# Kernel tuning notes

Measured on AMD Instinct MI355X. Metric: run time of the kernel, lower is better.

Reference implementation:

```python
import jax, jax.numpy as jnp
import numpy as np

EPS = 1e-3  # keras LayerNormalization default epsilon

def _layernorm(x, g, b):
    mu = jnp.mean(x, axis=-1, keepdims=True)
    var = jnp.mean(jnp.square(x - mu), axis=-1, keepdims=True)
    return (x - mu) * jax.lax.rsqrt(var + EPS) * g + b

def setup_inputs() -> dict:
    key = jax.random.key(0)
    ks = jax.random.split(key, 12)
    B, T, C = 2, 2048, 768
    s = 0.02
    return {
        "x": jax.random.normal(ks[0], (B, T, C), jnp.float32),
        "ln1_g": jnp.ones((C,), jnp.float32), "ln1_b": jnp.zeros((C,), jnp.float32),
        "Wq": jax.random.normal(ks[1], (C, C), jnp.float32) * s, "bq": jnp.zeros((C,), jnp.float32),
        "Wk": jax.random.normal(ks[2], (C, C), jnp.float32) * s, "bk": jnp.zeros((C,), jnp.float32),
        "Wv": jax.random.normal(ks[3], (C, C), jnp.float32) * s, "bv": jnp.zeros((C,), jnp.float32),
        "ln2_g": jnp.ones((C,), jnp.float32), "ln2_b": jnp.zeros((C,), jnp.float32),
        "W1": jax.random.normal(ks[4], (C, 4 * C), jnp.float32) * s, "b1": jnp.zeros((4 * C,), jnp.float32),
        "W2": jax.random.normal(ks[5], (4 * C, C), jnp.float32) * s, "b2": jnp.zeros((C,), jnp.float32),
    }

def reference(x, ln1_g, ln1_b, Wq, bq, Wk, bk, Wv, bv, ln2_g, ln2_b, W1, b1, W2, b2):
    H = 12
    B, T, C = x.shape
    dh = C // H
    # pre-LN (note: original overwrites x with LN output before residual)
    x = _layernorm(x, ln1_g, ln1_b)
    q = (x @ Wq + bq).reshape(B, T, H, dh).transpose(0, 2, 1, 3)
    k = (x @ Wk + bk).reshape(B, T, H, dh).transpose(0, 2, 1, 3)
    v = (x @ Wv + bv).reshape(B, T, H, dh).transpose(0, 2, 1, 3)
    # original computes K @ Q^T (transpose_b on query)
    scores = jnp.einsum('bhid,bhjd->bhij', k, q) / jnp.sqrt(jnp.float32(dh))
    mask = jnp.tril(jnp.ones((T, T), bool))
    scores = jnp.where(mask, scores, -jnp.inf)
    p = jax.nn.softmax(scores, axis=-1)
    y = jnp.einsum('bhij,bhjd->bhid', p, v)  # [B,H,T,dh]
    y = y.transpose(0, 2, 1, 3).reshape(B, T, C)
    x = x + y
    h = _layernorm(x, ln2_g, ln2_b)
    h = jax.nn.gelu(h @ W1 + b1, approximate=False)
    h = h @ W2 + b2
    return x + h
```

## Files before the change

### kernel.cpp

```cpp
#include <hip/hip_runtime.h>
#include <hip/hip_bf16.h>
#include <cmath>


#define BB 2
#define TT 2048
#define CC 768
#define HH 12
#define DH 64
#define NROWS (BB*TT)
#define NHEADS (BB*HH)

typedef __attribute__((ext_vector_type(8))) short bf16x8;
typedef __attribute__((ext_vector_type(4))) float f32x4;
typedef __attribute__((ext_vector_type(4))) unsigned short u16x4;

__device__ __forceinline__ unsigned short f2bf(float f){
  union { __hip_bfloat16 h; unsigned short u; } c;
  c.h = __float2bfloat16(f);
  return c.u;
}
__device__ __forceinline__ float bf2f(unsigned short u){
  union { unsigned int i; float f; } x; x.i = ((unsigned int)u) << 16; return x.f;
}
template<int BK>
__device__ __forceinline__ int swzk(int r, int c){
  if constexpr (BK == 64) return (r << 6) + (c ^ ((r & 7) << 3));
  else                    return (r << 5) + (c ^ (((r >> 1) & 3) << 3));
}
template<int BK>
__device__ __forceinline__ int swzsrc(int r, int c){
  if constexpr (BK == 64) return c ^ ((r & 7) << 3);
  else                    return c ^ (((r >> 1) & 3) << 3);
}
__device__ __forceinline__ float wred_sum(float v){
  #pragma unroll
  for(int m = 1; m < 64; m <<= 1) v += __shfl_xor(v, m, 64);
  return v;
}
__device__ __forceinline__ float gelu_fast(float x){
  float x2 = x * x;
  float e = x * fmaf(x2, 0.044715f, 1.0f) * 2.30203136f;
  float t = exp2f(e);
  return x - x / (t + 1.0f);
}
__device__ __forceinline__ void gload_lds16(const void* g, void* l){
  __builtin_amdgcn_global_load_lds((const __attribute__((address_space(1))) void*)g,
                                   (__attribute__((address_space(3))) void*)l, 16, 0, 0);
}
template<int N> __device__ __forceinline__ void waitcnt_vm(){
  if constexpr (N == 0)      asm volatile("s_waitcnt vmcnt(0)" ::: "memory");
  else if constexpr (N == 4) asm volatile("s_waitcnt vmcnt(4)" ::: "memory");
  else if constexpr (N == 8) asm volatile("s_waitcnt vmcnt(8)" ::: "memory");
  else static_assert(N == 0 || N == 4 || N == 8, "unsupported vmcnt");
}

#define SCLOG2 (0.125f * 1.44269504f)

__device__ __forceinline__ void tc_body(const float* __restrict__ in,
                                        unsigned short* __restrict__ out,
                                        int K, int N, int bx, int by,
                                        float (*tile)[33]){
  int n0 = bx * 32, k0 = by * 32;
  int t = threadIdx.x;
  int r = t >> 3, c4 = (t & 7) * 4;
  *(float4*)&tile[r][c4] = *(const float4*)&in[(size_t)(k0 + r) * N + n0 + c4];
  __syncthreads();
  u16x4 pk;
  #pragma unroll
  for(int j = 0; j < 4; j++) pk[j] = f2bf(tile[c4 + j][r]);
  *(u16x4*)&out[(size_t)(n0 + r) * K + k0 + c4] = pk;
}

__device__ __forceinline__ void ln_body(const float* __restrict__ in,
                                        const float* __restrict__ gm,
                                        const float* __restrict__ bt,
                                        unsigned short* __restrict__ out_b,
                                        int r){
  int t = threadIdx.x;
  const float* row = in + (size_t)r * CC;
  float v0 = row[t], v1 = row[t + 256], v2 = row[t + 512];
  float s = wred_sum(v0 + v1 + v2);
  __shared__ float red[4];
  if((t & 63) == 0) red[t >> 6] = s;
  __syncthreads();
  float mu = (red[0] + red[1] + red[2] + red[3]) * (1.0f / CC);
  float d0 = v0 - mu, d1 = v1 - mu, d2 = v2 - mu;
  float q = wred_sum(d0 * d0 + d1 * d1 + d2 * d2);
  __shared__ float red2[4];
  if((t & 63) == 0) red2[t >> 6] = q;
  __syncthreads();
  float var = (red2[0] + red2[1] + red2[2] + red2[3]) * (1.0f / CC);
  float rinv = rsqrtf(var + 1e-3f);
  float o0 = d0 * rinv * gm[t]       + bt[t];
  float o1 = d1 * rinv * gm[t + 256] + bt[t + 256];
  float o2 = d2 * rinv * gm[t + 512] + bt[t + 512];
  size_t base = (size_t)r * CC;
  out_b[base + t] = f2bf(o0); out_b[base + t + 256] = f2bf(o1); out_b[base + t + 512] = f2bf(o2);
}

__global__ __launch_bounds__(256) void prep_ln_kernel(const float* __restrict__ Wq,
                                                      const float* __restrict__ Wk,
                                                      const float* __restrict__ Wv,
                                                      const float* __restrict__ W1,
                                                      const float* __restrict__ W2,
                                                      const float* __restrict__ bq,
                                                      const float* __restrict__ bk,
                                                      const float* __restrict__ bv,
                                                      const float* __restrict__ x,
                                                      const float* __restrict__ ln1g,
                                                      const float* __restrict__ ln1b,
                                                      unsigned short* __restrict__ wqkv,
                                                      unsigned short* __restrict__ w1t,
                                                      unsigned short* __restrict__ w2t,
                                                      float* __restrict__ bqkv,
                                                      unsigned short* __restrict__ xlnb){
  __shared__ float tile[32][33];
  int o = blockIdx.x;
  if(o < 1728){
    int z = o / 576, r = o % 576;
    const float* in = (z == 0) ? Wq : (z == 1) ? Wk : Wv;
    tc_body(in, wqkv + (size_t)z * CC * CC, CC, CC, r % 24, r / 24, tile);
  } else if(o < 4032){
    int r = o - 1728;
    tc_body(W1, w1t, CC, 4 * CC, r % 96, r / 96, tile);
  } else if(o < 6336){
    int r = o - 4032;
    tc_body(W2, w2t, 4 * CC, CC, r % 24, r / 24, tile);
  } else if(o < 6345){
    int i = (o - 6336) * 256 + threadIdx.x;
    if(i < 3 * CC) bqkv[i] = (i < CC) ? bq[i] : (i < 2 * CC) ? bk[i - CC] : bv[i - 2 * CC];
  } else {
    ln_body(x, ln1g, ln1b, xlnb, o - 6345);
  }
}

template<int MODE, int TILE, int BK>
__global__ __launch_bounds__(256) void gemm_bt(const unsigned short* __restrict__ A,
                                               const unsigned short* __restrict__ Bt,
                                               const float* __restrict__ bias,
                                               const float* __restrict__ resid,
                                               void* __restrict__ outp,
                                               unsigned short* __restrict__ vt,
                                               int M, int N, int K){
  constexpr int F = TILE / 32;
  constexpr int SEGS = TILE * BK / 512;
  constexpr int R = SEGS / 4;
  constexpr int NLD = 2 * R;
  constexpr int LPR = BK / 8;
  constexpr int RPS = 512 / BK;
  __shared__ unsigned short As[3][TILE * BK];
  __shared__ unsigned short Bs[3][TILE * BK];
  int nb = gridDim.x, mbL = gridDim.y >> 3;
  int flat = blockIdx.y * nb + blockIdx.x;
  int xcd = flat & 7, sfl = flat >> 3;
  int by = xcd * mbL + sfl / nb;
  int bx = sfl % nb;
  int m0 = by * TILE, n0 = bx * TILE;
  int t = threadIdx.x; int w = t >> 6; int l = t & 63;
  int g = l >> 4; int lc = l & 15;
  int wm = w >> 1, wn = w & 1;
  f32x4 zero4 = {0.f, 0.f, 0.f, 0.f};
  f32x4 acc[F][F];
  #pragma unroll
  for(int mi = 0; mi < F; mi++)
    #pragma unroll
    for(int ni = 0; ni < F; ni++) acc[mi][ni] = zero4;

  auto stage = [&](int ks, int cb){
    #pragma unroll
    for(int p = 0; p < R; p++){
      int sgi = w * R + p;
      int r = sgi * RPS + l / LPR;
      int c = (l % LPR) * 8;
      int csrc = swzsrc<BK>(r, c);
      gload_lds16(A  + (size_t)(m0 + r) * K + ks + csrc, &As[cb][sgi * 512]);
      gload_lds16(Bt + (size_t)(n0 + r) * K + ks + csrc, &Bs[cb][sgi * 512]);
    }
  };

  int nt = K / BK;
  stage(0, 0);
  if(nt > 1) stage(BK, 1);
  if(nt > 2) stage(2 * BK, 2);
  int cur = 0;
  for(int ti = 0; ti < nt; ti++){
    if(ti + 2 < nt)      waitcnt_vm<2 * NLD>();
    else if(ti + 1 < nt) waitcnt_vm<NLD>();
    else                 waitcnt_vm<0>();
    __builtin_amdgcn_s_barrier();
    #pragma unroll
    for(int kk = 0; kk < BK / 32; kk++){
      bf16x8 af[F], bfv[F];
      #pragma unroll
      for(int mi = 0; mi < F; mi++) af[mi]  = *(const bf16x8*)&As[cur][swzk<BK>(wm * (TILE / 2) + mi * 16 + lc, kk * 32 + g * 8)];
      #pragma unroll
      for(int ni = 0; ni < F; ni++) bfv[ni] = *(const bf16x8*)&Bs[cur][swzk<BK>(wn * (TILE / 2) + ni * 16 + lc, kk * 32 + g * 8)];
      #pragma unroll
      for(int mi = 0; mi < F; mi++)
        #pragma unroll
        for(int ni = 0; ni < F; ni++)
          acc[mi][ni] = __builtin_amdgcn_mfma_f32_16x16x32_bf16(af[mi], bfv[ni], acc[mi][ni], 0, 0, 0);
    }
    __builtin_amdgcn_s_barrier();
    if(ti + 3 < nt) stage((ti + 3) * BK, cur);
    cur = (cur == 2) ? 0 : cur + 1;
  }
  #pragma unroll
  for(int mi = 0; mi < F; mi++)
    #pragma unroll
    for(int ni = 0; ni < F; ni++){
      int col = n0 + wn * (TILE / 2) + ni * 16 + lc;
      float bvv = bias[col];
      if(MODE == 3 && col >= 2 * CC){
        int hh = (col - 2 * CC) >> 6, d = (col - 2 * CC) & 63;
        int rowb = m0 + wm * (TILE / 2) + mi * 16 + g * 4;
        int bb = rowb >> 11, tb = rowb & 2047;
        u16x4 pk;
        #pragma unroll
        for(int rr = 0; rr < 4; rr++) pk[rr] = f2bf(acc[mi][ni][rr] + bvv);
        *(u16x4*)&vt[(((size_t)bb * HH + hh) * DH + d) * TT + tb] = pk;
      } else {
        #pragma unroll
        for(int rr = 0; rr < 4; rr++){
          int row = m0 + wm * (TILE / 2) + mi * 16 + g * 4 + rr;
          float v = acc[mi][ni][rr] + bvv;
          size_t idx = (size_t)row * N + col;
          if(MODE == 1) v = gelu_fast(v);
          if(MODE == 2) ((float*)outp)[idx] = v + resid[idx];
          else          ((unsigned short*)outp)[idx] = f2bf(v);
        }
      }
    }
}

__global__ __launch_bounds__(256) void attn_kernel(const unsigned short* __restrict__ qkv,
                                                   const unsigned short* __restrict__ vt,
                                                   unsigned short* __restrict__ po,
                                                   float* __restrict__ pl,
                                                   float* __restrict__ pm){
  __shared__ unsigned short Aq[2][64 * 64];
  __shared__ unsigned short Vs[2][64 * 64];
  __shared__ unsigned short Ps[4][16 * 64];
  int o = blockIdx.x;
  int xcd = o & 7, qq = o >> 3;
  int head = xcd * 3 + (qq % 3);
  int r_ = qq / 3;
  int bx = 31 - (r_ >> 1);
  int sp = r_ & 1;
  int b = head / HH, h = head % HH;
  int t = threadIdx.x; int w = t >> 6; int l = t & 63;
  int g = l >> 4, lc = l & 15;
  int i0w = bx * 64 + w * 16;
  int irow = i0w + lc;
  unsigned short* pw = &Ps[w][0];

  int hh = (bx + 2) >> 1;
  int js0 = sp ? hh : 0;
  int js1 = sp ? (bx + 1) : hh;

  int rl = l >> 3;
  int csrc = ((l & 7) * 8) ^ (rl * 8);

  bf16x8 bk[2];
  #pragma unroll
  for(int kk = 0; kk < 2; kk++)
    bk[kk] = *(const bf16x8*)(qkv + (size_t)(b * TT + irow) * (3 * CC) + CC + h * DH + kk * 32 + g * 8);

  float m_ = 0.0f, lsum = 0.f;
  f32x4 zero4 = {0.f, 0.f, 0.f, 0.f};
  f32x4 o4[4];
  #pragma unroll
  for(int ds = 0; ds < 4; ds++) o4[ds] = zero4;

  auto stage = [&](int j0, int cb){
    #pragma unroll
    for(int p = 0; p < 2; p++){
      int sgi = w * 2 + p;
      int row = sgi * 8 + rl;
      gload_lds16(qkv + (size_t)(b * TT + j0 + row) * (3 * CC) + h * DH + csrc, &Aq[cb][sgi * 512]);
      gload_lds16(vt  + (size_t)(head * DH + row) * TT + j0 + csrc,             &Vs[cb][sgi * 512]);
    }
  };

  if(js0 < js1){
    stage(js0 * 64, js0 & 1);
    if(js0 + 1 < js1) stage((js0 + 1) * 64, (js0 + 1) & 1);

    for(int jt = js0; jt < js1; jt++){
      int j0 = jt * 64;
      int buf = jt & 1;
      if(jt + 1 < js1) waitcnt_vm<4>(); else waitcnt_vm<0>();
      __builtin_amdgcn_s_barrier();
      f32x4 s[4];
      __builtin_amdgcn_s_setprio(1);
      #pragma unroll
      for(int js = 0; js < 4; js++){
        s[js] = zero4;
        #pragma unroll
        for(int kk = 0; kk < 2; kk++){
          bf16x8 aq = *(const bf16x8*)&Aq[buf][swzk<64>(js * 16 + lc, kk * 32 + g * 8)];
          s[js] = __builtin_amdgcn_mfma_f32_16x16x32_bf16(aq, bk[kk], s[js], 0, 0, 0);
        }
      }
      __builtin_amdgcn_s_setprio(0);
      if(j0 + 63 > i0w){
        #pragma unroll
        for(int js = 0; js < 4; js++)
          #pragma unroll
          for(int rr = 0; rr < 4; rr++){
            int j = j0 + js * 16 + g * 4 + rr;
            if(j > irow) s[js][rr] = -1e30f;
          }
      }
      float nmSC = -m_ * SCLOG2;
      f32x4 p[4];
      float rsum = 0.f;
      #pragma unroll
      for(int js = 0; js < 4; js++)
        #pragma unroll
        for(int rr = 0; rr < 4; rr++){
          float pv = exp2f(fmaf(s[js][rr], SCLOG2, nmSC));
          p[js][rr] = pv;
          rsum += pv;
        }
      rsum += __shfl_xor(rsum, 16, 64);
      rsum += __shfl_xor(rsum, 32, 64);
      if(__builtin_expect(__any(!(rsum < 1e30f)), 0)){
        float mx = -1e30f;
        #pragma unroll
        for(int js = 0; js < 4; js++)
          #pragma unroll
          for(int rr = 0; rr < 4; rr++) mx = fmaxf(mx, s[js][rr]);
        mx = fmaxf(mx, __shfl_xor(mx, 16, 64));
        mx = fmaxf(mx, __shfl_xor(mx, 32, 64));
        float mn = fmaxf(m_, mx);
        float al = exp2f((m_ - mn) * SCLOG2);
        m_ = mn;
        lsum *= al;
        #pragma unroll
        for(int rr = 0; rr < 4; rr++){
          float alb = __shfl(al, g * 4 + rr, 64);
          #pragma unroll
          for(int ds = 0; ds < 4; ds++) o4[ds][rr] *= alb;
        }
        nmSC = -m_ * SCLOG2;
        rsum = 0.f;
        #pragma unroll
        for(int js = 0; js < 4; js++)
          #pragma unroll
          for(int rr = 0; rr < 4; rr++){
            float pv = exp2f(fmaf(s[js][rr], SCLOG2, nmSC));
            p[js][rr] = pv;
            rsum += pv;
          }
        rsum += __shfl_xor(rsum, 16, 64);
        rsum += __shfl_xor(rsum, 32, 64);
      }
      lsum += rsum;
      #pragma unroll
      for(int js = 0; js < 4; js++){
        u16x4 pk;
        #pragma unroll
        for(int rr = 0; rr < 4; rr++) pk[rr] = f2bf(p[js][rr]);
        *(u16x4*)&pw[swzk<64>(lc, js * 16 + g * 4)] = pk;
      }
      bf16x8 pa[2];
      #pragma unroll
      for(int kk = 0; kk < 2; kk++)
        pa[kk] = *(const bf16x8*)&pw[swzk<64>(lc, kk * 32 + g * 8)];
      __builtin_amdgcn_s_setprio(1);
      #pragma unroll
      for(int ds = 0; ds < 4; ds++)
        #pragma unroll
        for(int kk = 0; kk < 2; kk++){
          bf16x8 vb = *(const bf16x8*)&Vs[buf][swzk<64>(ds * 16 + lc, kk * 32 + g * 8)];
          o4[ds] = __builtin_amdgcn_mfma_f32_16x16x32_bf16(pa[kk], vb, o4[ds], 0, 0, 0);
        }
      __builtin_amdgcn_s_setprio(0);
      __builtin_amdgcn_s_barrier();
      if(jt + 2 < js1) stage((jt + 2) * 64, buf);
    }
  }
  size_t pobase = (size_t)sp * (NHEADS * TT * DH) + (size_t)head * TT * DH;
  #pragma unroll
  for(int rr = 0; rr < 4; rr++){
    int ig = i0w + g * 4 + rr;
    #pragma unroll
    for(int ds = 0; ds < 4; ds++)
      po[pobase + (size_t)ig * DH + ds * 16 + lc] = f2bf(o4[ds][rr]);
  }
  if(g == 0){
    size_t pidx = (size_t)sp * (NHEADS * TT) + (size_t)head * TT + i0w + lc;
    pl[pidx] = lsum;
    pm[pidx] = m_;
  }
}

__global__ __launch_bounds__(256) void combine_ln2(const unsigned short* __restrict__ po,
                                                   const float* __restrict__ pl,
                                                   const float* __restrict__ pm,
                                                   const unsigned short* __restrict__ xlnb,
                                                   const float* __restrict__ gm,
                                                   const float* __restrict__ bt,
                                                   float* __restrict__ x1,
                                                   unsigned short* __restrict__ hln2){
  int r = blockIdx.x; int t = threadIdx.x;
  int b = r >> 11, i = r & 2047;
  float v[3];
  #pragma unroll
  for(int p = 0; p < 3; p++){
    int c = t + p * 256;
    int h = c >> 6, d = c & 63;
    size_t pidx = ((size_t)(b * HH + h)) * TT + i;
    float m0v = pm[pidx], m1v = pm[pidx + NHEADS * TT];
    float l0 = pl[pidx],  l1 = pl[pidx + NHEADS * TT];
    float M = fmaxf(m0v, m1v);
    float w0 = exp2f((m0v - M) * SCLOG2), w1 = exp2f((m1v - M) * SCLOG2);
    float p0 = bf2f(po[pidx * DH + d]);
    float p1 = bf2f(po[(size_t)NHEADS * TT * DH + pidx * DH + d]);
    float att = (p0 * w0 + p1 * w1) / (l0 * w0 + l1 * w1);
    v[p] = bf2f(xlnb[(size_t)r * CC + c]) + att;
  }
  float s = wred_sum(v[0] + v[1] + v[2]);
  __shared__ float red[4];
  if((t & 63) == 0) red[t >> 6] = s;
  __syncthreads();
  float mu = (red[0] + red[1] + red[2] + red[3]) * (1.0f / CC);
  float d0 = v[0] - mu, d1 = v[1] - mu, d2 = v[2] - mu;
  float q = wred_sum(d0 * d0 + d1 * d1 + d2 * d2);
  __shared__ float red2[4];
  if((t & 63) == 0) red2[t >> 6] = q;
  __syncthreads();
  float var = (red2[0] + red2[1] + red2[2] + red2[3]) * (1.0f / CC);
  float rinv = rsqrtf(var + 1e-3f);
  size_t base = (size_t)r * CC;
  x1[base + t] = v[0]; x1[base + t + 256] = v[1]; x1[base + t + 512] = v[2];
  hln2[base + t]       = f2bf(d0 * rinv * gm[t]       + bt[t]);
  hln2[base + t + 256] = f2bf(d1 * rinv * gm[t + 256] + bt[t + 256]);
  hln2[base + t + 512] = f2bf(d2 * rinv * gm[t + 512] + bt[t + 512]);
}

extern "C" void kernel_launch(void* const* d_in, const int* in_sizes, int n_in,
                              void* d_out, int out_size, void* d_ws, size_t ws_size,
                              hipStream_t stream){
  const float* x    = (const float*)d_in[0];
  const float* ln1g = (const float*)d_in[1];
  const float* ln1b = (const float*)d_in[2];
  const float* Wq   = (const float*)d_in[3];
  const float* bq   = (const float*)d_in[4];
  const float* Wk   = (const float*)d_in[5];
  const float* bk   = (const float*)d_in[6];
  const float* Wv   = (const float*)d_in[7];
  const float* bv   = (const float*)d_in[8];
  const float* ln2g = (const float*)d_in[9];
  const float* ln2b = (const float*)d_in[10];
  const float* W1   = (const float*)d_in[11];
  const float* b1   = (const float*)d_in[12];
  const float* W2   = (const float*)d_in[13];
  const float* b2   = (const float*)d_in[14];

  char* ws = (char*)d_ws;
  unsigned short* po   = (unsigned short*)(ws + 0);
  unsigned short* xlnb = (unsigned short*)(ws + 12582912);
  float*          x1   = (float*)(ws + 18874368);
  unsigned short* hln2 = (unsigned short*)(ws + 31457280);
  unsigned short* wqkv = (unsigned short*)(ws + 37748736);
  float*          bqkv = (float*)(ws + 41287680);
  unsigned short* w1t  = (unsigned short*)(ws + 41296896);
  unsigned short* w2t  = (unsigned short*)(ws + 46015488);
  unsigned short* qkv  = (unsigned short*)(ws + 50734080);
  unsigned short* vt   = (unsigned short*)(ws + 69608448);
  float*          pl   = (float*)(ws + 75899904);
  float*          pm   = (float*)(ws + 76293120);
  unsigned short* mlp1 = (unsigned short*)(ws + 50734080);

  prep_ln_kernel<<<dim3(6345 + NROWS), 256, 0, stream>>>(Wq, Wk, Wv, W1, W2, bq, bk, bv,
                                                         x, ln1g, ln1b,
                                                         wqkv, w1t, w2t, bqkv, xlnb);

  gemm_bt<3, 128, 32><<<dim3(18, 32), 256, 0, stream>>>(xlnb, wqkv, bqkv, nullptr, qkv, vt, NROWS, 3 * CC, CC);

  attn_kernel<<<dim3(1536), 256, 0, stream>>>(qkv, vt, po, pl, pm);

  combine_ln2<<<dim3(NROWS), 256, 0, stream>>>(po, pl, pm, xlnb, ln2g, ln2b, x1, hln2);

  gemm_bt<1, 128, 32><<<dim3(24, 32), 256, 0, stream>>>(hln2, w1t, b1, nullptr, mlp1, nullptr, NROWS, 4 * CC, CC);

  gemm_bt<2, 64, 64><<<dim3(12, 64), 256, 0, stream>>>(mlp1, w2t, b2, x1, d_out, nullptr, NROWS, CC, 4 * CC);

  (void)in_sizes; (void)n_in; (void)out_size; (void)ws_size;
}
```

Measured before the change: 149.0 us.

## Replace 4-wave GEMM with single-wave 128x64 tile GEMM without block barriers

The templated 256-thread GEMM with triple-buffered LDS and block barriers is replaced by a 64-thread, one-wavefront kernel. Each wave computes a 128x64 output tile with double-buffered async global-to-LDS loads and an 8x4 MFMA accumulator array. With a single wave per block no s_barrier is needed, so workgroup synchronization cost is removed and more independent blocks can be resident. The trade-off is higher register pressure, fewer tile rows shared across waves, and only double buffering. The W2 GEMM grid drops to 384 blocks, which may leave compute units underused.

```diff
diff --git a/kernel.cpp b/kernel.cpp
--- a/kernel.cpp
+++ b/kernel.cpp
@@ -49,10 +49,10 @@
                                    (__attribute__((address_space(3))) void*)l, 16, 0, 0);
 }
 template<int N> __device__ __forceinline__ void waitcnt_vm(){
-  if constexpr (N == 0)      asm volatile("s_waitcnt vmcnt(0)" ::: "memory");
-  else if constexpr (N == 4) asm volatile("s_waitcnt vmcnt(4)" ::: "memory");
-  else if constexpr (N == 8) asm volatile("s_waitcnt vmcnt(8)" ::: "memory");
-  else static_assert(N == 0 || N == 4 || N == 8, "unsupported vmcnt");
+  if constexpr (N == 0)       asm volatile("s_waitcnt vmcnt(0)" ::: "memory");
+  else if constexpr (N == 4)  asm volatile("s_waitcnt vmcnt(4)" ::: "memory");
+  else if constexpr (N == 12) asm volatile("s_waitcnt vmcnt(12)" ::: "memory");
+  else static_assert(N == 0 || N == 4 || N == 12, "unsupported vmcnt");
 }
 
 #define SCLOG2 (0.125f * 1.44269504f)
@@ -135,86 +135,75 @@
   }
 }
 
-template<int MODE, int TILE, int BK>
-__global__ __launch_bounds__(256) void gemm_bt(const unsigned short* __restrict__ A,
-                                               const unsigned short* __restrict__ Bt,
-                                               const float* __restrict__ bias,
-                                               const float* __restrict__ resid,
-                                               void* __restrict__ outp,
-                                               unsigned short* __restrict__ vt,
-                                               int M, int N, int K){
-  constexpr int F = TILE / 32;
-  constexpr int SEGS = TILE * BK / 512;
-  constexpr int R = SEGS / 4;
-  constexpr int NLD = 2 * R;
-  constexpr int LPR = BK / 8;
-  constexpr int RPS = 512 / BK;
-  __shared__ unsigned short As[3][TILE * BK];
-  __shared__ unsigned short Bs[3][TILE * BK];
+template<int MODE>
+__global__ __launch_bounds__(64) void gemm_1w(const unsigned short* __restrict__ A,
+                                              const unsigned short* __restrict__ Bt,
+                                              const float* __restrict__ bias,
+                                              const float* __restrict__ resid,
+                                              void* __restrict__ outp,
+                                              unsigned short* __restrict__ vt,
+                                              int M, int N, int K){
+  __shared__ unsigned short As[2][128 * 32];
+  __shared__ unsigned short Bs[2][64 * 32];
   int nb = gridDim.x, mbL = gridDim.y >> 3;
   int flat = blockIdx.y * nb + blockIdx.x;
   int xcd = flat & 7, sfl = flat >> 3;
   int by = xcd * mbL + sfl / nb;
   int bx = sfl % nb;
-  int m0 = by * TILE, n0 = bx * TILE;
-  int t = threadIdx.x; int w = t >> 6; int l = t & 63;
-  int g = l >> 4; int lc = l & 15;
-  int wm = w >> 1, wn = w & 1;
+  int m0 = by * 128, n0 = bx * 64;
+  int l = threadIdx.x; int g = l >> 4, lc = l & 15;
   f32x4 zero4 = {0.f, 0.f, 0.f, 0.f};
-  f32x4 acc[F][F];
-  #pragma unroll
-  for(int mi = 0; mi < F; mi++)
-    #pragma unroll
-    for(int ni = 0; ni < F; ni++) acc[mi][ni] = zero4;
-
+  f32x4 acc[8][4];
+  #pragma unroll
+  for(int mi = 0; mi < 8; mi++)
+    #pragma unroll
+    for(int ni = 0; ni < 4; ni++) acc[mi][ni] = zero4;
+
+  int rsg = l >> 2, csg = (l & 3) * 8;
   auto stage = [&](int ks, int cb){
     #pragma unroll
-    for(int p = 0; p < R; p++){
-      int sgi = w * R + p;
-      int r = sgi * RPS + l / LPR;
-      int c = (l % LPR) * 8;
-      int csrc = swzsrc<BK>(r, c);
-      gload_lds16(A  + (size_t)(m0 + r) * K + ks + csrc, &As[cb][sgi * 512]);
-      gload_lds16(Bt + (size_t)(n0 + r) * K + ks + csrc, &Bs[cb][sgi * 512]);
+    for(int s = 0; s < 8; s++){
+      int r = s * 16 + rsg;
+      int csrc = csg ^ (((r >> 1) & 3) << 3);
+      gload_lds16(A + (size_t)(m0 + r) * K + ks + csrc, &As[cb][s * 512]);
+    }
+    #pragma unroll
+    for(int s = 0; s < 4; s++){
+      int r = s * 16 + rsg;
+      int csrc = csg ^ (((r >> 1) & 3) << 3);
+      gload_lds16(Bt + (size_t)(n0 + r) * K + ks + csrc, &Bs[cb][s * 512]);
     }
   };
 
-  int nt = K / BK;
+  int nt = K >> 5;
   stage(0, 0);
-  if(nt > 1) stage(BK, 1);
-  if(nt > 2) stage(2 * BK, 2);
-  int cur = 0;
+  stage(32, 1);
   for(int ti = 0; ti < nt; ti++){
-    if(ti + 2 < nt)      waitcnt_vm<2 * NLD>();
-    else if(ti + 1 < nt) waitcnt_vm<NLD>();
-    else                 waitcnt_vm<0>();
-    __builtin_amdgcn_s_barrier();
-    #pragma unroll
-    for(int kk = 0; kk < BK / 32; kk++){
-      bf16x8 af[F], bfv[F];
-      #pragma unroll
-      for(int mi = 0; mi < F; mi++) af[mi]  = *(const bf16x8*)&As[cur][swzk<BK>(wm * (TILE / 2) + mi * 16 + lc, kk * 32 + g * 8)];
-      #pragma unroll
-      for(int ni = 0; ni < F; ni++) bfv[ni] = *(const bf16x8*)&Bs[cur][swzk<BK>(wn * (TILE / 2) + ni * 16 + lc, kk * 32 + g * 8)];
-      #pragma unroll
-      for(int mi = 0; mi < F; mi++)
-        #pragma unroll
-        for(int ni = 0; ni < F; ni++)
-          acc[mi][ni] = __builtin_amdgcn_mfma_f32_16x16x32_bf16(af[mi], bfv[ni], acc[mi][ni], 0, 0, 0);
-    }
-    __builtin_amdgcn_s_barrier();
-    if(ti + 3 < nt) stage((ti + 3) * BK, cur);
-    cur = (cur == 2) ? 0 : cur + 1;
-  }
-  #pragma unroll
-  for(int mi = 0; mi < F; mi++)
-    #pragma unroll
-    for(int ni = 0; ni < F; ni++){
-      int col = n0 + wn * (TILE / 2) + ni * 16 + lc;
+    if(ti + 1 < nt) waitcnt_vm<12>(); else waitcnt_vm<0>();
+    int cur = ti & 1;
+    bf16x8 af[8], bfv[4];
+    #pragma unroll
+    for(int mi = 0; mi < 8; mi++) af[mi]  = *(const bf16x8*)&As[cur][swzk<32>(mi * 16 + lc, g * 8)];
+    #pragma unroll
+    for(int ni = 0; ni < 4; ni++) bfv[ni] = *(const bf16x8*)&Bs[cur][swzk<32>(ni * 16 + lc, g * 8)];
+    #pragma unroll
+    for(int mi = 0; mi < 8; mi++)
+      #pragma unroll
+      for(int ni = 0; ni < 4; ni++)
+        acc[mi][ni] = __builtin_amdgcn_mfma_f32_16x16x32_bf16(af[mi], bfv[ni], acc[mi][ni], 0, 0, 0);
+    asm volatile("s_waitcnt lgkmcnt(0)" ::: "memory");
+    __builtin_amdgcn_sched_barrier(0);
+    if(ti + 2 < nt) stage((ti + 2) * 32, cur);
+  }
+  #pragma unroll
+  for(int mi = 0; mi < 8; mi++)
+    #pragma unroll
+    for(int ni = 0; ni < 4; ni++){
+      int col = n0 + ni * 16 + lc;
       float bvv = bias[col];
       if(MODE == 3 && col >= 2 * CC){
         int hh = (col - 2 * CC) >> 6, d = (col - 2 * CC) & 63;
-        int rowb = m0 + wm * (TILE / 2) + mi * 16 + g * 4;
+        int rowb = m0 + mi * 16 + g * 4;
         int bb = rowb >> 11, tb = rowb & 2047;
         u16x4 pk;
         #pragma unroll
@@ -223,7 +212,7 @@
       } else {
         #pragma unroll
         for(int rr = 0; rr < 4; rr++){
-          int row = m0 + wm * (TILE / 2) + mi * 16 + g * 4 + rr;
+          int row = m0 + mi * 16 + g * 4 + rr;
           float v = acc[mi][ni][rr] + bvv;
           size_t idx = (size_t)row * N + col;
           if(MODE == 1) v = gelu_fast(v);
@@ -479,15 +468,15 @@
                                                          x, ln1g, ln1b,
                                                          wqkv, w1t, w2t, bqkv, xlnb);
 
-  gemm_bt<3, 128, 32><<<dim3(18, 32), 256, 0, stream>>>(xlnb, wqkv, bqkv, nullptr, qkv, vt, NROWS, 3 * CC, CC);
+  gemm_1w<3><<<dim3(36, 32), 64, 0, stream>>>(xlnb, wqkv, bqkv, nullptr, qkv, vt, NROWS, 3 * CC, CC);
 
   attn_kernel<<<dim3(1536), 256, 0, stream>>>(qkv, vt, po, pl, pm);
 
   combine_ln2<<<dim3(NROWS), 256, 0, stream>>>(po, pl, pm, xlnb, ln2g, ln2b, x1, hln2);
 
-  gemm_bt<1, 128, 32><<<dim3(24, 32), 256, 0, stream>>>(hln2, w1t, b1, nullptr, mlp1, nullptr, NROWS, 4 * CC, CC);
-
-  gemm_bt<2, 64, 64><<<dim3(12, 64), 256, 0, stream>>>(mlp1, w2t, b2, x1, d_out, nullptr, NROWS, CC, 4 * CC);
+  gemm_1w<1><<<dim3(48, 32), 64, 0, stream>>>(hln2, w1t, b1, nullptr, mlp1, nullptr, NROWS, 4 * CC, CC);
+
+  gemm_1w<2><<<dim3(12, 32), 64, 0, stream>>>(mlp1, w2t, b2, x1, d_out, nullptr, NROWS, CC, 4 * CC);
 
   (void)in_sizes; (void)n_in; (void)out_size; (void)ws_size;
 }
```

Result: slower. 232.4 us (+55.9%).
